# Optimization experiments

Hardware: AMD Instinct MI355X
Metric: run time of the kernel (lower is better)

Reference implementation:

```python
import jax, jax.numpy as jnp
import numpy as np

N_NODES = 50000
N_EDGES = 1_250_000
D_FEAT = 64


def setup_inputs() -> dict:
    key = jax.random.key(0)
    k1, k2, k3 = jax.random.split(key, 3)
    graph_embedding = jax.random.normal(k1, (N_NODES, D_FEAT), dtype=jnp.float32)
    src = jax.random.randint(k2, (N_EDGES,), 0, N_NODES, dtype=jnp.int64)
    dst = jax.random.randint(k3, (N_EDGES,), 0, N_NODES, dtype=jnp.int64)
    return {"graph_embedding": graph_embedding, "src": src, "dst": dst}


def reference(graph_embedding, src, dst):
    # DGL update_all(copy_u('ft','m'), sum('m','ft')):
    # out[v] = sum over edges (u->v) of graph_embedding[u]
    messages = graph_embedding[src]  # [E, d] gather
    out = jax.ops.segment_sum(messages, dst, num_segments=graph_embedding.shape[0])
    return out
```

## Files before the change

### kernel.cpp

```cpp
#include <hip/hip_runtime.h>


#define D_FEAT 64
#define NB2    512
#define CAPB   3072
#define MAXNB  512
#define PCHUNK 8192
#define CAP1   96

static __device__ __forceinline__ unsigned short f2bf(float f) {
    unsigned u = __float_as_uint(f);
    u += 0x7fffu + ((u >> 16) & 1u);
    return (unsigned short)(u >> 16);
}

__global__ __launch_bounds__(1024) void fused_cvt_partition_kernel(
    const float4* __restrict__ emb4,
    uint2*        __restrict__ embh2,
    const int*    __restrict__ src,
    const int*    __restrict__ dst,
    unsigned*     __restrict__ cursor,
    unsigned*     __restrict__ packed,
    int n4, int p_blocks, int n_edges, unsigned npb_inv)
{
    __shared__ unsigned lhist[MAXNB];
    __shared__ unsigned lbase[MAXNB];

    if ((int)blockIdx.x >= p_blocks) {
        int cb = blockIdx.x - p_blocks;
        int base = cb * 4096 + (int)threadIdx.x;
        #pragma unroll
        for (int r = 0; r < 4; ++r) {
            int i = base + r * 1024;
            if (i < n4) {
                float4 x = emb4[i];
                uint2 o;
                o.x = (unsigned)f2bf(x.x) | ((unsigned)f2bf(x.y) << 16);
                o.y = (unsigned)f2bf(x.z) | ((unsigned)f2bf(x.w) << 16);
                embh2[i] = o;
            }
        }
        return;
    }

    int pb   = blockIdx.x;
    int t    = threadIdx.x;
    int base = pb * PCHUNK;
    int cnt  = n_edges - base; if (cnt > PCHUNK) cnt = PCHUNK; if (cnt < 0) cnt = 0;

    for (int i = t; i < MAXNB; i += 1024) lhist[i] = 0;
    __syncthreads();

    int nv = cnt >> 2;
    const int4* d4 = (const int4*)(dst + base);
    const int4* s4 = (const int4*)(src + base);
    int  i0 = t, i1 = t + 1024;
    bool f0 = i0 < nv, f1 = i1 < nv;
    uint4 pa, pb4;
    if (f0) {
        int4 d = d4[i0]; int4 s = s4[i0];
        pa.x = ((unsigned)d.x << 16) | (unsigned)s.x;
        pa.y = ((unsigned)d.y << 16) | (unsigned)s.y;
        pa.z = ((unsigned)d.z << 16) | (unsigned)s.z;
        pa.w = ((unsigned)d.w << 16) | (unsigned)s.w;
    }
    if (f1) {
        int4 d = d4[i1]; int4 s = s4[i1];
        pb4.x = ((unsigned)d.x << 16) | (unsigned)s.x;
        pb4.y = ((unsigned)d.y << 16) | (unsigned)s.y;
        pb4.z = ((unsigned)d.z << 16) | (unsigned)s.z;
        pb4.w = ((unsigned)d.w << 16) | (unsigned)s.w;
    }
    if (f0) {
        atomicAdd(&lhist[__umulhi(pa.x >> 16, npb_inv)], 1u);
        atomicAdd(&lhist[__umulhi(pa.y >> 16, npb_inv)], 1u);
        atomicAdd(&lhist[__umulhi(pa.z >> 16, npb_inv)], 1u);
        atomicAdd(&lhist[__umulhi(pa.w >> 16, npb_inv)], 1u);
    }
    if (f1) {
        atomicAdd(&lhist[__umulhi(pb4.x >> 16, npb_inv)], 1u);
        atomicAdd(&lhist[__umulhi(pb4.y >> 16, npb_inv)], 1u);
        atomicAdd(&lhist[__umulhi(pb4.z >> 16, npb_inv)], 1u);
        atomicAdd(&lhist[__umulhi(pb4.w >> 16, npb_inv)], 1u);
    }
    for (int i = nv * 4 + t; i < cnt; i += 1024)
        atomicAdd(&lhist[__umulhi((unsigned)dst[base + i], npb_inv)], 1u);
    __syncthreads();

    for (int i = t; i < MAXNB; i += 1024) {
        unsigned c = lhist[i];
        lbase[i] = c ? atomicAdd(&cursor[i], c) : 0u;
        lhist[i] = 0;
    }
    __syncthreads();

    #define SCAT(p) { \
        unsigned b_ = __umulhi((p) >> 16, npb_inv); \
        unsigned pos_ = lbase[b_] + atomicAdd(&lhist[b_], 1u); \
        if (pos_ < CAPB) packed[(size_t)b_ * CAPB + pos_] = (p); }
    if (f0) { SCAT(pa.x); SCAT(pa.y); SCAT(pa.z); SCAT(pa.w); }
    if (f1) { SCAT(pb4.x); SCAT(pb4.y); SCAT(pb4.z); SCAT(pb4.w); }
    for (int i = nv * 4 + t; i < cnt; i += 1024) {
        unsigned p = ((unsigned)dst[base + i] << 16) | (unsigned)src[base + i];
        SCAT(p);
    }
    #undef SCAT
}

#define ACC8(h) \
    a0 += __uint_as_float(h.x << 16);           \
    a1 += __uint_as_float(h.x & 0xffff0000u);   \
    a2 += __uint_as_float(h.y << 16);           \
    a3 += __uint_as_float(h.y & 0xffff0000u);   \
    a4 += __uint_as_float(h.z << 16);           \
    a5 += __uint_as_float(h.z & 0xffff0000u);   \
    a6 += __uint_as_float(h.w << 16);           \
    a7 += __uint_as_float(h.w & 0xffff0000u);

__global__ __launch_bounds__(1024, 8) void sortgather_kernel(
    const unsigned short* __restrict__ embh,
    const unsigned*       __restrict__ cursor,
    const unsigned*       __restrict__ packed,
    float*                __restrict__ out,
    int n_nodes, unsigned npb)
{
    __shared__ unsigned       lpk[CAPB];
    __shared__ unsigned short slist[CAPB];
    __shared__ unsigned       hist[128];
    __shared__ unsigned       cur[128];
    __shared__ unsigned       stc[128];

    int b = blockIdx.x;
    int t = threadIdx.x;
    int node_base = (int)(b * npb);
    int nn = n_nodes - node_base;
    if (nn > (int)npb) nn = (int)npb;
    if (nn < 0) nn = 0;

    int cnt = (int)cursor[b]; if (cnt > CAPB) cnt = CAPB;
    const unsigned* pk = packed + (size_t)b * CAPB;

    if (t < 128) hist[t] = 0;
    __syncthreads();

    for (int i = t; i < cnt; i += 1024) {
        unsigned p = pk[i];
        lpk[i] = p;
        atomicAdd(&hist[(p >> 16) - node_base], 1u);
    }
    __syncthreads();

    if (t < 64) {
        int l = t;
        unsigned v0 = hist[2 * l], v1 = hist[2 * l + 1];
        unsigned s = v0 + v1;
        unsigned inc = s;
        #pragma unroll
        for (int d = 1; d < 64; d <<= 1) {
            unsigned u = __shfl_up(inc, d);
            if (l >= d) inc += u;
        }
        unsigned exc = inc - s;
        cur[2 * l]     = exc;
        cur[2 * l + 1] = exc + v0;
        stc[2 * l]     = (exc << 16) | v0;
        stc[2 * l + 1] = ((exc + v0) << 16) | v1;
    }
    __syncthreads();

    for (int i = t; i < cnt; i += 1024) {
        unsigned p = lpk[i];
        unsigned pos = atomicAdd(&cur[(p >> 16) - node_base], 1u);
        slist[pos] = (unsigned short)(p & 0xffffu);
    }
    __syncthreads();

    int g  = t >> 3;
    int l8 = t & 7;

    unsigned sc = stc[g];
    int st = (int)(sc >> 16), cn = (int)(sc & 0xffffu);

    float a0=0.f,a1=0.f,a2=0.f,a3=0.f,a4=0.f,a5=0.f,a6=0.f,a7=0.f;

    for (int j = 0; j < cn; j += 8) {
        bool v1 = j + 1 < cn, v2 = j + 2 < cn, v3 = j + 3 < cn;
        bool v4 = j + 4 < cn, v5 = j + 5 < cn, v6 = j + 6 < cn, v7 = j + 7 < cn;
        uint4 h0, h1, h2, h3, h4, h5, h6, h7;
        h0 =          *(const uint4*)(embh + ((size_t)slist[st + j    ] << 6) + l8 * 8);
        if (v1) h1 =  *(const uint4*)(embh + ((size_t)slist[st + j + 1] << 6) + l8 * 8);
        if (v2) h2 =  *(const uint4*)(embh + ((size_t)slist[st + j + 2] << 6) + l8 * 8);
        if (v3) h3 =  *(const uint4*)(embh + ((size_t)slist[st + j + 3] << 6) + l8 * 8);
        if (v4) h4 =  *(const uint4*)(embh + ((size_t)slist[st + j + 4] << 6) + l8 * 8);
        if (v5) h5 =  *(const uint4*)(embh + ((size_t)slist[st + j + 5] << 6) + l8 * 8);
        if (v6) h6 =  *(const uint4*)(embh + ((size_t)slist[st + j + 6] << 6) + l8 * 8);
        if (v7) h7 =  *(const uint4*)(embh + ((size_t)slist[st + j + 7] << 6) + l8 * 8);
        { ACC8(h0); }
        if (v1) { ACC8(h1); }
        if (v2) { ACC8(h2); }
        if (v3) { ACC8(h3); }
        if (v4) { ACC8(h4); }
        if (v5) { ACC8(h5); }
        if (v6) { ACC8(h6); }
        if (v7) { ACC8(h7); }
    }

    if (g < nn) {
        float4* o4 = (float4*)(out + (size_t)(node_base + g) * D_FEAT + l8 * 8);
        o4[0] = make_float4(a0, a1, a2, a3);
        o4[1] = make_float4(a4, a5, a6, a7);
    }
}

__global__ __launch_bounds__(256) void count_scatter_kernel(
    const int* __restrict__ src, const int* __restrict__ dst,
    int* __restrict__ cnt, int* __restrict__ bucket, int n_edges)
{
    int e = blockIdx.x * blockDim.x + threadIdx.x;
    if (e >= n_edges) return;
    int s = src[e], d = dst[e];
    int pos = atomicAdd(&cnt[d], 1);
    if (pos < CAP1) bucket[(size_t)d * CAP1 + pos] = s;
}

__global__ __launch_bounds__(256) void gather_sum_kernel(
    const float* __restrict__ emb, const int* __restrict__ cnt,
    const int* __restrict__ bucket, float* __restrict__ out, int n_nodes)
{
    int v = (blockIdx.x * blockDim.x + threadIdx.x) >> 6;
    int lane = threadIdx.x & 63;
    if (v >= n_nodes) return;
    int n = cnt[v]; if (n > CAP1) n = CAP1;
    const int* b = bucket + (size_t)v * CAP1;
    float acc = 0.f;
    for (int j = 0; j < n; ++j)
        acc += emb[(size_t)b[j] * D_FEAT + lane];
    out[(size_t)v * D_FEAT + lane] = acc;
}

__global__ __launch_bounds__(256) void scatter_sum_fallback(
    const float* __restrict__ emb, const int* __restrict__ src,
    const int* __restrict__ dst, float* __restrict__ out, int n_edges)
{
    int gid = blockIdx.x * blockDim.x + threadIdx.x;
    int e = gid >> 4;
    if (e >= n_edges) return;
    int c = gid & 15;
    int s = src[e], d = dst[e];
    const float4* emb4 = (const float4*)emb;
    float4 v = emb4[(size_t)s * 16 + c];
    float* o = out + (size_t)d * D_FEAT + c * 4;
    atomicAdd(o + 0, v.x); atomicAdd(o + 1, v.y);
    atomicAdd(o + 2, v.z); atomicAdd(o + 3, v.w);
}

extern "C" void kernel_launch(void* const* d_in, const int* in_sizes, int n_in,
                              void* d_out, int out_size, void* d_ws, size_t ws_size,
                              hipStream_t stream) {
    const float* emb = (const float*)d_in[0];
    const int*   src = (const int*)d_in[1];
    const int*   dst = (const int*)d_in[2];
    float*       out = (float*)d_out;

    int n_edges = in_sizes[1];
    int n_nodes = out_size / D_FEAT;

    unsigned npb = (unsigned)((n_nodes + NB2 - 1) / NB2);
    if (npb == 0) npb = 1;
    int nb = (n_nodes + (int)npb - 1) / (int)npb;
    unsigned npb_inv = (unsigned)((0x100000000ULL + npb - 1) / npb);

    size_t cur_b  = 4096;
    size_t pack_b = (size_t)MAXNB * CAPB * sizeof(unsigned);
    size_t embh_b = (size_t)n_nodes * D_FEAT * sizeof(unsigned short);

    if (n_nodes <= 65536 && npb <= 128 && nb <= MAXNB &&
        ws_size >= cur_b + pack_b + embh_b) {
        char* p = (char*)d_ws;
        unsigned*       cursor = (unsigned*)p;        p += cur_b;
        unsigned*       packed = (unsigned*)p;        p += pack_b;
        unsigned short* embh   = (unsigned short*)p;

        hipMemsetAsync(cursor, 0, (size_t)MAXNB * sizeof(unsigned), stream);

        int n4 = n_nodes * D_FEAT / 4;
        int p_blocks   = (n_edges + PCHUNK - 1) / PCHUNK;
        int cvt_blocks = (n4 + 4095) / 4096;
        fused_cvt_partition_kernel<<<p_blocks + cvt_blocks, 1024, 0, stream>>>(
            (const float4*)emb, (uint2*)embh, src, dst, cursor, packed,
            n4, p_blocks, n_edges, npb_inv);

        sortgather_kernel<<<nb, 1024, 0, stream>>>(
            embh, cursor, packed, out, n_nodes, npb);
    } else if (ws_size >= (size_t)n_nodes * sizeof(int) * (1 + CAP1)) {
        int* cnt    = (int*)d_ws;
        int* bucket = (int*)((char*)d_ws + (size_t)n_nodes * sizeof(int));
        hipMemsetAsync(cnt, 0, (size_t)n_nodes * sizeof(int), stream);
        count_scatter_kernel<<<(n_edges + 255) / 256, 256, 0, stream>>>(
            src, dst, cnt, bucket, n_edges);
        gather_sum_kernel<<<(n_nodes * 64 + 255) / 256, 256, 0, stream>>>(
            emb, cnt, bucket, out, n_nodes);
    } else {
        hipMemsetAsync(d_out, 0, (size_t)out_size * sizeof(float), stream);
        long long total = (long long)n_edges * 16;
        scatter_sum_fallback<<<(int)((total + 255) / 256), 256, 0, stream>>>(
            emb, src, dst, out, n_edges);
    }
}
```

Before: 100.8 us.

## Split bf16 table into feature halves and use per-XCD partition cursors

The bf16 embedding table is stored as two half-feature tables, and each gather block now handles one 32-feature half of a node bucket with 512 threads. Block indices are mapped so that blocks sharing a half-table are meant to land on the same XCD, shrinking the per-XCD L2 working set. The partition step also keeps eight separate cursor and packed segments, chosen by partition block index, to spread global atomic contention. The cost is that every gather block re-sorts its bucket redundantly, which doubles the sort work, and it adds a CAPSEG overflow risk per segment.

New measurement: 105.3 us. 4.5% more time.

```diff
diff --git a/kernel.cpp b/kernel.cpp
--- a/kernel.cpp
+++ b/kernel.cpp
@@ -4,7 +4,9 @@
 #define D_FEAT 64
 #define NB2    512
 #define CAPB   3072
+#define CAPSEG 1024
 #define MAXNB  512
+#define NXCD   8
 #define PCHUNK 8192
 #define CAP1   96
 
@@ -37,16 +39,23 @@
                 uint2 o;
                 o.x = (unsigned)f2bf(x.x) | ((unsigned)f2bf(x.y) << 16);
                 o.y = (unsigned)f2bf(x.z) | ((unsigned)f2bf(x.w) << 16);
-                embh2[i] = o;
+                int n = i >> 4;
+                int q = i & 15;
+                uint2* tb = embh2 + ((q & 8) ? (n4 >> 1) : 0);
+                tb[n * 8 + (q & 7)] = o;
             }
         }
         return;
     }
 
     int pb   = blockIdx.x;
+    int my_x = pb & (NXCD - 1);
     int t    = threadIdx.x;
     int base = pb * PCHUNK;
     int cnt  = n_edges - base; if (cnt > PCHUNK) cnt = PCHUNK; if (cnt < 0) cnt = 0;
+
+    unsigned* my_cur = cursor + my_x * MAXNB;
+    unsigned* my_pk  = packed + (size_t)my_x * MAXNB * CAPSEG;
 
     for (int i = t; i < MAXNB; i += 1024) lhist[i] = 0;
     __syncthreads();
@@ -89,7 +98,7 @@
 
     for (int i = t; i < MAXNB; i += 1024) {
         unsigned c = lhist[i];
-        lbase[i] = c ? atomicAdd(&cursor[i], c) : 0u;
+        lbase[i] = c ? atomicAdd(&my_cur[i], c) : 0u;
         lhist[i] = 0;
     }
     __syncthreads();
@@ -97,7 +106,7 @@
     #define SCAT(p) { \
         unsigned b_ = __umulhi((p) >> 16, npb_inv); \
         unsigned pos_ = lbase[b_] + atomicAdd(&lhist[b_], 1u); \
-        if (pos_ < CAPB) packed[(size_t)b_ * CAPB + pos_] = (p); }
+        if (pos_ < CAPSEG) my_pk[(size_t)b_ * CAPSEG + pos_] = (p); }
     if (f0) { SCAT(pa.x); SCAT(pa.y); SCAT(pa.z); SCAT(pa.w); }
     if (f1) { SCAT(pb4.x); SCAT(pb4.y); SCAT(pb4.z); SCAT(pb4.w); }
     for (int i = nv * 4 + t; i < cnt; i += 1024) {
@@ -117,36 +126,57 @@
     a6 += __uint_as_float(h.w << 16);           \
     a7 += __uint_as_float(h.w & 0xffff0000u);
 
-__global__ __launch_bounds__(1024, 8) void sortgather_kernel(
+__global__ __launch_bounds__(512, 8) void sortgather_kernel(
     const unsigned short* __restrict__ embh,
     const unsigned*       __restrict__ cursor,
     const unsigned*       __restrict__ packed,
     float*                __restrict__ out,
-    int n_nodes, unsigned npb)
+    int n_nodes, unsigned npb, int nb)
 {
     __shared__ unsigned       lpk[CAPB];
     __shared__ unsigned short slist[CAPB];
     __shared__ unsigned       hist[128];
     __shared__ unsigned       cur[128];
     __shared__ unsigned       stc[128];
-
-    int b = blockIdx.x;
+    __shared__ unsigned       scnt[NXCD];
+    __shared__ unsigned       soff[NXCD + 1];
+
+    int k = blockIdx.x;
+    int b = (k >> 3) * 4 + (k & 3);
+    int h = (k >> 2) & 1;
+    if (b >= nb) return;
     int t = threadIdx.x;
     int node_base = (int)(b * npb);
     int nn = n_nodes - node_base;
     if (nn > (int)npb) nn = (int)npb;
     if (nn < 0) nn = 0;
 
-    int cnt = (int)cursor[b]; if (cnt > CAPB) cnt = CAPB;
-    const unsigned* pk = packed + (size_t)b * CAPB;
-
+    if (t < NXCD) {
+        unsigned c = cursor[t * MAXNB + b];
+        scnt[t] = c > CAPSEG ? CAPSEG : c;
+    }
     if (t < 128) hist[t] = 0;
     __syncthreads();
-
-    for (int i = t; i < cnt; i += 1024) {
-        unsigned p = pk[i];
-        lpk[i] = p;
-        atomicAdd(&hist[(p >> 16) - node_base], 1u);
+    if (t == 0) {
+        unsigned s = 0;
+        #pragma unroll
+        for (int x = 0; x < NXCD; ++x) { soff[x] = s; s += scnt[x]; }
+        soff[NXCD] = s;
+    }
+    __syncthreads();
+    int cnt = (int)soff[NXCD]; if (cnt > CAPB) cnt = CAPB;
+
+    for (int x = 0; x < NXCD; ++x) {
+        const unsigned* sp = packed + ((size_t)x * MAXNB + b) * CAPSEG;
+        int c = (int)scnt[x], o = (int)soff[x];
+        for (int i = t; i < c; i += 512) {
+            int pos = o + i;
+            if (pos < CAPB) {
+                unsigned p = sp[i];
+                lpk[pos] = p;
+                atomicAdd(&hist[(p >> 16) - node_base], 1u);
+            }
+        }
     }
     __syncthreads();
 
@@ -168,15 +198,16 @@
     }
     __syncthreads();
 
-    for (int i = t; i < cnt; i += 1024) {
+    for (int i = t; i < cnt; i += 512) {
         unsigned p = lpk[i];
         unsigned pos = atomicAdd(&cur[(p >> 16) - node_base], 1u);
         slist[pos] = (unsigned short)(p & 0xffffu);
     }
     __syncthreads();
 
-    int g  = t >> 3;
-    int l8 = t & 7;
+    const unsigned short* tb = embh + (size_t)h * ((size_t)n_nodes << 5);
+    int g  = t >> 2;
+    int l4 = t & 3;
 
     unsigned sc = stc[g];
     int st = (int)(sc >> 16), cn = (int)(sc & 0xffffu);
@@ -187,14 +218,14 @@
         bool v1 = j + 1 < cn, v2 = j + 2 < cn, v3 = j + 3 < cn;
         bool v4 = j + 4 < cn, v5 = j + 5 < cn, v6 = j + 6 < cn, v7 = j + 7 < cn;
         uint4 h0, h1, h2, h3, h4, h5, h6, h7;
-        h0 =          *(const uint4*)(embh + ((size_t)slist[st + j    ] << 6) + l8 * 8);
-        if (v1) h1 =  *(const uint4*)(embh + ((size_t)slist[st + j + 1] << 6) + l8 * 8);
-        if (v2) h2 =  *(const uint4*)(embh + ((size_t)slist[st + j + 2] << 6) + l8 * 8);
-        if (v3) h3 =  *(const uint4*)(embh + ((size_t)slist[st + j + 3] << 6) + l8 * 8);
-        if (v4) h4 =  *(const uint4*)(embh + ((size_t)slist[st + j + 4] << 6) + l8 * 8);
-        if (v5) h5 =  *(const uint4*)(embh + ((size_t)slist[st + j + 5] << 6) + l8 * 8);
-        if (v6) h6 =  *(const uint4*)(embh + ((size_t)slist[st + j + 6] << 6) + l8 * 8);
-        if (v7) h7 =  *(const uint4*)(embh + ((size_t)slist[st + j + 7] << 6) + l8 * 8);
+        h0 =          *(const uint4*)(tb + ((size_t)slist[st + j    ] << 5) + l4 * 8);
+        if (v1) h1 =  *(const uint4*)(tb + ((size_t)slist[st + j + 1] << 5) + l4 * 8);
+        if (v2) h2 =  *(const uint4*)(tb + ((size_t)slist[st + j + 2] << 5) + l4 * 8);
+        if (v3) h3 =  *(const uint4*)(tb + ((size_t)slist[st + j + 3] << 5) + l4 * 8);
+        if (v4) h4 =  *(const uint4*)(tb + ((size_t)slist[st + j + 4] << 5) + l4 * 8);
+        if (v5) h5 =  *(const uint4*)(tb + ((size_t)slist[st + j + 5] << 5) + l4 * 8);
+        if (v6) h6 =  *(const uint4*)(tb + ((size_t)slist[st + j + 6] << 5) + l4 * 8);
+        if (v7) h7 =  *(const uint4*)(tb + ((size_t)slist[st + j + 7] << 5) + l4 * 8);
         { ACC8(h0); }
         if (v1) { ACC8(h1); }
         if (v2) { ACC8(h2); }
@@ -206,7 +237,7 @@
     }
 
     if (g < nn) {
-        float4* o4 = (float4*)(out + (size_t)(node_base + g) * D_FEAT + l8 * 8);
+        float4* o4 = (float4*)(out + (size_t)(node_base + g) * D_FEAT + h * 32 + l4 * 8);
         o4[0] = make_float4(a0, a1, a2, a3);
         o4[1] = make_float4(a4, a5, a6, a7);
     }
@@ -270,8 +301,8 @@
     int nb = (n_nodes + (int)npb - 1) / (int)npb;
     unsigned npb_inv = (unsigned)((0x100000000ULL + npb - 1) / npb);
 
-    size_t cur_b  = 4096;
-    size_t pack_b = (size_t)MAXNB * CAPB * sizeof(unsigned);
+    size_t cur_b  = (size_t)NXCD * MAXNB * sizeof(unsigned);
+    size_t pack_b = (size_t)NXCD * MAXNB * CAPSEG * sizeof(unsigned);
     size_t embh_b = (size_t)n_nodes * D_FEAT * sizeof(unsigned short);
 
     if (n_nodes <= 65536 && npb <= 128 && nb <= MAXNB &&
@@ -281,7 +312,7 @@
         unsigned*       packed = (unsigned*)p;        p += pack_b;
         unsigned short* embh   = (unsigned short*)p;
 
-        hipMemsetAsync(cursor, 0, (size_t)MAXNB * sizeof(unsigned), stream);
+        hipMemsetAsync(cursor, 0, cur_b, stream);
 
         int n4 = n_nodes * D_FEAT / 4;
         int p_blocks   = (n_edges + PCHUNK - 1) / PCHUNK;
@@ -290,8 +321,9 @@
             (const float4*)emb, (uint2*)embh, src, dst, cursor, packed,
             n4, p_blocks, n_edges, npb_inv);
 
-        sortgather_kernel<<<nb, 1024, 0, stream>>>(
-            embh, cursor, packed, out, n_nodes, npb);
+        int g_blocks = ((nb + 3) / 4) * 8;
+        sortgather_kernel<<<g_blocks, 512, 0, stream>>>(
+            embh, cursor, packed, out, n_nodes, npb, nb);
     } else if (ws_size >= (size_t)n_nodes * sizeof(int) * (1 + CAP1)) {
         int* cnt    = (int*)d_ws;
         int* bucket = (int*)((char*)d_ws + (size_t)n_nodes * sizeof(int));
```

## Replace global atomic bucket cursors with per-block fixed slabs in edge partitioning

Applied to the files above, without the earlier changes.

The partition kernel no longer builds a block-local histogram and reserves space with global atomics on a shared cursor array. Each partition block now writes edges straight into its own fixed 64-entry slab per destination bucket and records per-block counts. The gather kernel prefix-sums those counts across partition blocks to compact the slabs into shared memory. This removes the memset launch, a histogram pass, one barrier and the global atomic contention. In exchange the workspace grows, the gather kernel reads sparse, mostly empty slabs, and edges are silently dropped if any bucket gets more than 64 edges from one chunk.

Result: slower. 103.5 us (+2.7%).

```diff
diff --git a/kernel.cpp b/kernel.cpp
--- a/kernel.cpp
+++ b/kernel.cpp
@@ -1,12 +1,15 @@
 #include <hip/hip_runtime.h>
 
 
-#define D_FEAT 64
-#define NB2    512
-#define CAPB   3072
-#define MAXNB  512
-#define PCHUNK 8192
-#define CAP1   96
+#define D_FEAT  64
+#define NB2     512
+#define CAPB    3072
+#define SLAB    64
+#define SLABLOG 6
+#define MAXNB   512
+#define MAXSEG  256
+#define PCHUNK  8192
+#define CAP1    96
 
 static __device__ __forceinline__ unsigned short f2bf(float f) {
     unsigned u = __float_as_uint(f);
@@ -19,12 +22,11 @@
     uint2*        __restrict__ embh2,
     const int*    __restrict__ src,
     const int*    __restrict__ dst,
-    unsigned*     __restrict__ cursor,
+    unsigned*     __restrict__ cnt_out,
     unsigned*     __restrict__ packed,
     int n4, int p_blocks, int n_edges, unsigned npb_inv)
 {
-    __shared__ unsigned lhist[MAXNB];
-    __shared__ unsigned lbase[MAXNB];
+    __shared__ unsigned cur[MAXNB];
 
     if ((int)blockIdx.x >= p_blocks) {
         int cb = blockIdx.x - p_blocks;
@@ -48,63 +50,45 @@
     int base = pb * PCHUNK;
     int cnt  = n_edges - base; if (cnt > PCHUNK) cnt = PCHUNK; if (cnt < 0) cnt = 0;
 
-    for (int i = t; i < MAXNB; i += 1024) lhist[i] = 0;
-    __syncthreads();
+    for (int i = t; i < MAXNB; i += 1024) cur[i] = 0;
+    __syncthreads();
+
+    unsigned* my_pk = packed + ((size_t)pb * MAXNB << SLABLOG);
+
+    #define SCAT(p) { \
+        unsigned b_ = __umulhi((p) >> 16, npb_inv); \
+        unsigned pos_ = atomicAdd(&cur[b_], 1u); \
+        if (pos_ < SLAB) my_pk[((size_t)b_ << SLABLOG) + pos_] = (p); }
 
     int nv = cnt >> 2;
     const int4* d4 = (const int4*)(dst + base);
     const int4* s4 = (const int4*)(src + base);
     int  i0 = t, i1 = t + 1024;
-    bool f0 = i0 < nv, f1 = i1 < nv;
-    uint4 pa, pb4;
-    if (f0) {
+    if (i0 < nv) {
         int4 d = d4[i0]; int4 s = s4[i0];
-        pa.x = ((unsigned)d.x << 16) | (unsigned)s.x;
-        pa.y = ((unsigned)d.y << 16) | (unsigned)s.y;
-        pa.z = ((unsigned)d.z << 16) | (unsigned)s.z;
-        pa.w = ((unsigned)d.w << 16) | (unsigned)s.w;
-    }
-    if (f1) {
+        unsigned p0 = ((unsigned)d.x << 16) | (unsigned)s.x;
+        unsigned p1 = ((unsigned)d.y << 16) | (unsigned)s.y;
+        unsigned p2 = ((unsigned)d.z << 16) | (unsigned)s.z;
+        unsigned p3 = ((unsigned)d.w << 16) | (unsigned)s.w;
+        SCAT(p0); SCAT(p1); SCAT(p2); SCAT(p3);
+    }
+    if (i1 < nv) {
         int4 d = d4[i1]; int4 s = s4[i1];
-        pb4.x = ((unsigned)d.x << 16) | (unsigned)s.x;
-        pb4.y = ((unsigned)d.y << 16) | (unsigned)s.y;
-        pb4.z = ((unsigned)d.z << 16) | (unsigned)s.z;
-        pb4.w = ((unsigned)d.w << 16) | (unsigned)s.w;
-    }
-    if (f0) {
-        atomicAdd(&lhist[__umulhi(pa.x >> 16, npb_inv)], 1u);
-        atomicAdd(&lhist[__umulhi(pa.y >> 16, npb_inv)], 1u);
-        atomicAdd(&lhist[__umulhi(pa.z >> 16, npb_inv)], 1u);
-        atomicAdd(&lhist[__umulhi(pa.w >> 16, npb_inv)], 1u);
-    }
-    if (f1) {
-        atomicAdd(&lhist[__umulhi(pb4.x >> 16, npb_inv)], 1u);
-        atomicAdd(&lhist[__umulhi(pb4.y >> 16, npb_inv)], 1u);
-        atomicAdd(&lhist[__umulhi(pb4.z >> 16, npb_inv)], 1u);
-        atomicAdd(&lhist[__umulhi(pb4.w >> 16, npb_inv)], 1u);
-    }
-    for (int i = nv * 4 + t; i < cnt; i += 1024)
-        atomicAdd(&lhist[__umulhi((unsigned)dst[base + i], npb_inv)], 1u);
-    __syncthreads();
-
-    for (int i = t; i < MAXNB; i += 1024) {
-        unsigned c = lhist[i];
-        lbase[i] = c ? atomicAdd(&cursor[i], c) : 0u;
-        lhist[i] = 0;
-    }
-    __syncthreads();
-
-    #define SCAT(p) { \
-        unsigned b_ = __umulhi((p) >> 16, npb_inv); \
-        unsigned pos_ = lbase[b_] + atomicAdd(&lhist[b_], 1u); \
-        if (pos_ < CAPB) packed[(size_t)b_ * CAPB + pos_] = (p); }
-    if (f0) { SCAT(pa.x); SCAT(pa.y); SCAT(pa.z); SCAT(pa.w); }
-    if (f1) { SCAT(pb4.x); SCAT(pb4.y); SCAT(pb4.z); SCAT(pb4.w); }
+        unsigned p0 = ((unsigned)d.x << 16) | (unsigned)s.x;
+        unsigned p1 = ((unsigned)d.y << 16) | (unsigned)s.y;
+        unsigned p2 = ((unsigned)d.z << 16) | (unsigned)s.z;
+        unsigned p3 = ((unsigned)d.w << 16) | (unsigned)s.w;
+        SCAT(p0); SCAT(p1); SCAT(p2); SCAT(p3);
+    }
     for (int i = nv * 4 + t; i < cnt; i += 1024) {
         unsigned p = ((unsigned)dst[base + i] << 16) | (unsigned)src[base + i];
         SCAT(p);
     }
     #undef SCAT
+    __syncthreads();
+
+    for (int i = t; i < MAXNB; i += 1024)
+        cnt_out[(size_t)pb * MAXNB + i] = cur[i];
 }
 
 #define ACC8(h) \
@@ -119,16 +103,19 @@
 
 __global__ __launch_bounds__(1024, 8) void sortgather_kernel(
     const unsigned short* __restrict__ embh,
-    const unsigned*       __restrict__ cursor,
+    const unsigned*       __restrict__ cnt,
     const unsigned*       __restrict__ packed,
     float*                __restrict__ out,
-    int n_nodes, unsigned npb)
+    int n_nodes, unsigned npb, int nseg)
 {
     __shared__ unsigned       lpk[CAPB];
     __shared__ unsigned short slist[CAPB];
     __shared__ unsigned       hist[128];
     __shared__ unsigned       cur[128];
     __shared__ unsigned       stc[128];
+    __shared__ unsigned       scnt[MAXSEG];
+    __shared__ unsigned       soff[MAXSEG];
+    __shared__ unsigned       stot;
 
     int b = blockIdx.x;
     int t = threadIdx.x;
@@ -137,16 +124,43 @@
     if (nn > (int)npb) nn = (int)npb;
     if (nn < 0) nn = 0;
 
-    int cnt = (int)cursor[b]; if (cnt > CAPB) cnt = CAPB;
-    const unsigned* pk = packed + (size_t)b * CAPB;
-
     if (t < 128) hist[t] = 0;
-    __syncthreads();
-
-    for (int i = t; i < cnt; i += 1024) {
-        unsigned p = pk[i];
-        lpk[i] = p;
-        atomicAdd(&hist[(p >> 16) - node_base], 1u);
+
+    if (t < 64) {
+        int x0 = t * 4;
+        unsigned c0=0,c1=0,c2=0,c3=0;
+        if (x0     < nseg) { unsigned c = cnt[(size_t)(x0    ) * MAXNB + b]; c0 = c > SLAB ? SLAB : c; }
+        if (x0 + 1 < nseg) { unsigned c = cnt[(size_t)(x0 + 1) * MAXNB + b]; c1 = c > SLAB ? SLAB : c; }
+        if (x0 + 2 < nseg) { unsigned c = cnt[(size_t)(x0 + 2) * MAXNB + b]; c2 = c > SLAB ? SLAB : c; }
+        if (x0 + 3 < nseg) { unsigned c = cnt[(size_t)(x0 + 3) * MAXNB + b]; c3 = c > SLAB ? SLAB : c; }
+        unsigned s = c0 + c1 + c2 + c3;
+        unsigned inc = s;
+        #pragma unroll
+        for (int d = 1; d < 64; d <<= 1) {
+            unsigned u = __shfl_up(inc, d);
+            if (t >= d) inc += u;
+        }
+        unsigned exc = inc - s;
+        scnt[x0] = c0;     soff[x0]     = exc;
+        scnt[x0+1] = c1;   soff[x0 + 1] = exc + c0;
+        scnt[x0+2] = c2;   soff[x0 + 2] = exc + c0 + c1;
+        scnt[x0+3] = c3;   soff[x0 + 3] = exc + c0 + c1 + c2;
+        if (t == 63) stot = inc;
+    }
+    __syncthreads();
+    int total = (int)stot; if (total > CAPB) total = CAPB;
+
+    int nslots = nseg << SLABLOG;
+    for (int i = t; i < nslots; i += 1024) {
+        int x = i >> SLABLOG, j = i & (SLAB - 1);
+        if ((unsigned)j < scnt[x]) {
+            unsigned p = packed[(((size_t)x * MAXNB + b) << SLABLOG) + j];
+            unsigned pos = soff[x] + j;
+            if (pos < CAPB) {
+                lpk[pos] = p;
+                atomicAdd(&hist[(p >> 16) - node_base], 1u);
+            }
+        }
     }
     __syncthreads();
 
@@ -168,7 +182,7 @@
     }
     __syncthreads();
 
-    for (int i = t; i < cnt; i += 1024) {
+    for (int i = t; i < total; i += 1024) {
         unsigned p = lpk[i];
         unsigned pos = atomicAdd(&cur[(p >> 16) - node_base], 1u);
         slist[pos] = (unsigned short)(p & 0xffffu);
@@ -270,28 +284,27 @@
     int nb = (n_nodes + (int)npb - 1) / (int)npb;
     unsigned npb_inv = (unsigned)((0x100000000ULL + npb - 1) / npb);
 
-    size_t cur_b  = 4096;
-    size_t pack_b = (size_t)MAXNB * CAPB * sizeof(unsigned);
+    int p_blocks = (n_edges + PCHUNK - 1) / PCHUNK;
+
+    size_t cnt_b  = (size_t)p_blocks * MAXNB * sizeof(unsigned);
+    size_t pack_b = ((size_t)p_blocks * MAXNB << SLABLOG) * sizeof(unsigned);
     size_t embh_b = (size_t)n_nodes * D_FEAT * sizeof(unsigned short);
 
-    if (n_nodes <= 65536 && npb <= 128 && nb <= MAXNB &&
-        ws_size >= cur_b + pack_b + embh_b) {
+    if (n_nodes <= 65536 && npb <= 128 && nb <= MAXNB && p_blocks <= MAXSEG &&
+        ws_size >= cnt_b + pack_b + embh_b) {
         char* p = (char*)d_ws;
-        unsigned*       cursor = (unsigned*)p;        p += cur_b;
+        unsigned*       cnt    = (unsigned*)p;        p += cnt_b;
         unsigned*       packed = (unsigned*)p;        p += pack_b;
         unsigned short* embh   = (unsigned short*)p;
 
-        hipMemsetAsync(cursor, 0, (size_t)MAXNB * sizeof(unsigned), stream);
-
         int n4 = n_nodes * D_FEAT / 4;
-        int p_blocks   = (n_edges + PCHUNK - 1) / PCHUNK;
         int cvt_blocks = (n4 + 4095) / 4096;
         fused_cvt_partition_kernel<<<p_blocks + cvt_blocks, 1024, 0, stream>>>(
-            (const float4*)emb, (uint2*)embh, src, dst, cursor, packed,
+            (const float4*)emb, (uint2*)embh, src, dst, cnt, packed,
             n4, p_blocks, n_edges, npb_inv);
 
         sortgather_kernel<<<nb, 1024, 0, stream>>>(
-            embh, cursor, packed, out, n_nodes, npb);
+            embh, cnt, packed, out, n_nodes, npb, p_blocks);
     } else if (ws_size >= (size_t)n_nodes * sizeof(int) * (1 + CAP1)) {
         int* cnt    = (int*)d_ws;
         int* bucket = (int*)((char*)d_ws + (size_t)n_nodes * sizeof(int));
```

## Replace block-partition sort with per-node global buckets and direct gather

Applied to the files above, without the earlier changes.

Drops the two-level partition, where edges were binned into node-range blocks and then counting-sorted in shared memory. Instead each edge is scattered straight into a fixed-capacity per-node bucket using global atomics on a per-node degree counter. The gather kernel reads neighbor ids directly from the bucket, prefetching them and broadcasting them with shuffles, and writes the output with nontemporal stores. This removes the shared-memory sort and its barriers, but adds 1.25M global atomics spread over 50k counters, scattered bucket writes, and a larger workspace footprint.

New measurement: 152.4 us. +51.2%, slower.

```diff
diff --git a/kernel.cpp b/kernel.cpp
--- a/kernel.cpp
+++ b/kernel.cpp
@@ -2,11 +2,8 @@
 
 
 #define D_FEAT 64
-#define NB2    512
-#define CAPB   3072
-#define MAXNB  512
+#define CAPN   96
 #define PCHUNK 8192
-#define CAP1   96
 
 static __device__ __forceinline__ unsigned short f2bf(float f) {
     unsigned u = __float_as_uint(f);
@@ -14,18 +11,17 @@
     return (unsigned short)(u >> 16);
 }
 
-__global__ __launch_bounds__(1024) void fused_cvt_partition_kernel(
+typedef float f4v __attribute__((ext_vector_type(4)));
+
+__global__ __launch_bounds__(1024) void fused_cvt_scatter_kernel(
     const float4* __restrict__ emb4,
     uint2*        __restrict__ embh2,
     const int*    __restrict__ src,
     const int*    __restrict__ dst,
-    unsigned*     __restrict__ cursor,
-    unsigned*     __restrict__ packed,
-    int n4, int p_blocks, int n_edges, unsigned npb_inv)
+    int*          __restrict__ deg,
+    int*          __restrict__ bucket,
+    int n4, int p_blocks, int n_edges)
 {
-    __shared__ unsigned lhist[MAXNB];
-    __shared__ unsigned lbase[MAXNB];
-
     if ((int)blockIdx.x >= p_blocks) {
         int cb = blockIdx.x - p_blocks;
         int base = cb * 4096 + (int)threadIdx.x;
@@ -43,67 +39,28 @@
         return;
     }
 
-    int pb   = blockIdx.x;
     int t    = threadIdx.x;
-    int base = pb * PCHUNK;
+    int base = blockIdx.x * PCHUNK;
     int cnt  = n_edges - base; if (cnt > PCHUNK) cnt = PCHUNK; if (cnt < 0) cnt = 0;
 
-    for (int i = t; i < MAXNB; i += 1024) lhist[i] = 0;
-    __syncthreads();
+    #define SCAT(d_, s_) { \
+        int pos_ = atomicAdd(&deg[d_], 1); \
+        if (pos_ < CAPN) bucket[(size_t)(d_) * CAPN + pos_] = (s_); }
 
     int nv = cnt >> 2;
     const int4* d4 = (const int4*)(dst + base);
     const int4* s4 = (const int4*)(src + base);
-    int  i0 = t, i1 = t + 1024;
-    bool f0 = i0 < nv, f1 = i1 < nv;
-    uint4 pa, pb4;
-    if (f0) {
+    int i0 = t, i1 = t + 1024;
+    if (i0 < nv) {
         int4 d = d4[i0]; int4 s = s4[i0];
-        pa.x = ((unsigned)d.x << 16) | (unsigned)s.x;
-        pa.y = ((unsigned)d.y << 16) | (unsigned)s.y;
-        pa.z = ((unsigned)d.z << 16) | (unsigned)s.z;
-        pa.w = ((unsigned)d.w << 16) | (unsigned)s.w;
+        SCAT(d.x, s.x); SCAT(d.y, s.y); SCAT(d.z, s.z); SCAT(d.w, s.w);
     }
-    if (f1) {
+    if (i1 < nv) {
         int4 d = d4[i1]; int4 s = s4[i1];
-        pb4.x = ((unsigned)d.x << 16) | (unsigned)s.x;
-        pb4.y = ((unsigned)d.y << 16) | (unsigned)s.y;
-        pb4.z = ((unsigned)d.z << 16) | (unsigned)s.z;
-        pb4.w = ((unsigned)d.w << 16) | (unsigned)s.w;
-    }
-    if (f0) {
-        atomicAdd(&lhist[__umulhi(pa.x >> 16, npb_inv)], 1u);
-        atomicAdd(&lhist[__umulhi(pa.y >> 16, npb_inv)], 1u);
-        atomicAdd(&lhist[__umulhi(pa.z >> 16, npb_inv)], 1u);
-        atomicAdd(&lhist[__umulhi(pa.w >> 16, npb_inv)], 1u);
-    }
-    if (f1) {
-        atomicAdd(&lhist[__umulhi(pb4.x >> 16, npb_inv)], 1u);
-        atomicAdd(&lhist[__umulhi(pb4.y >> 16, npb_inv)], 1u);
-        atomicAdd(&lhist[__umulhi(pb4.z >> 16, npb_inv)], 1u);
-        atomicAdd(&lhist[__umulhi(pb4.w >> 16, npb_inv)], 1u);
+        SCAT(d.x, s.x); SCAT(d.y, s.y); SCAT(d.z, s.z); SCAT(d.w, s.w);
     }
     for (int i = nv * 4 + t; i < cnt; i += 1024)
-        atomicAdd(&lhist[__umulhi((unsigned)dst[base + i], npb_inv)], 1u);
-    __syncthreads();
-
-    for (int i = t; i < MAXNB; i += 1024) {
-        unsigned c = lhist[i];
-        lbase[i] = c ? atomicAdd(&cursor[i], c) : 0u;
-        lhist[i] = 0;
-    }
-    __syncthreads();
-
-    #define SCAT(p) { \
-        unsigned b_ = __umulhi((p) >> 16, npb_inv); \
-        unsigned pos_ = lbase[b_] + atomicAdd(&lhist[b_], 1u); \
-        if (pos_ < CAPB) packed[(size_t)b_ * CAPB + pos_] = (p); }
-    if (f0) { SCAT(pa.x); SCAT(pa.y); SCAT(pa.z); SCAT(pa.w); }
-    if (f1) { SCAT(pb4.x); SCAT(pb4.y); SCAT(pb4.z); SCAT(pb4.w); }
-    for (int i = nv * 4 + t; i < cnt; i += 1024) {
-        unsigned p = ((unsigned)dst[base + i] << 16) | (unsigned)src[base + i];
-        SCAT(p);
-    }
+        SCAT(dst[base + i], src[base + i]);
     #undef SCAT
 }
 
@@ -117,84 +74,47 @@
     a6 += __uint_as_float(h.w << 16);           \
     a7 += __uint_as_float(h.w & 0xffff0000u);
 
-__global__ __launch_bounds__(1024, 8) void sortgather_kernel(
+__global__ __launch_bounds__(512, 8) void gather_kernel(
     const unsigned short* __restrict__ embh,
-    const unsigned*       __restrict__ cursor,
-    const unsigned*       __restrict__ packed,
+    const int*            __restrict__ deg,
+    const int*            __restrict__ bucket,
     float*                __restrict__ out,
-    int n_nodes, unsigned npb)
+    int n_nodes)
 {
-    __shared__ unsigned       lpk[CAPB];
-    __shared__ unsigned short slist[CAPB];
-    __shared__ unsigned       hist[128];
-    __shared__ unsigned       cur[128];
-    __shared__ unsigned       stc[128];
-
-    int b = blockIdx.x;
-    int t = threadIdx.x;
-    int node_base = (int)(b * npb);
-    int nn = n_nodes - node_base;
-    if (nn > (int)npb) nn = (int)npb;
-    if (nn < 0) nn = 0;
-
-    int cnt = (int)cursor[b]; if (cnt > CAPB) cnt = CAPB;
-    const unsigned* pk = packed + (size_t)b * CAPB;
-
-    if (t < 128) hist[t] = 0;
-    __syncthreads();
-
-    for (int i = t; i < cnt; i += 1024) {
-        unsigned p = pk[i];
-        lpk[i] = p;
-        atomicAdd(&hist[(p >> 16) - node_base], 1u);
-    }
-    __syncthreads();
-
-    if (t < 64) {
-        int l = t;
-        unsigned v0 = hist[2 * l], v1 = hist[2 * l + 1];
-        unsigned s = v0 + v1;
-        unsigned inc = s;
-        #pragma unroll
-        for (int d = 1; d < 64; d <<= 1) {
-            unsigned u = __shfl_up(inc, d);
-            if (l >= d) inc += u;
-        }
-        unsigned exc = inc - s;
-        cur[2 * l]     = exc;
-        cur[2 * l + 1] = exc + v0;
-        stc[2 * l]     = (exc << 16) | v0;
-        stc[2 * l + 1] = ((exc + v0) << 16) | v1;
-    }
-    __syncthreads();
-
-    for (int i = t; i < cnt; i += 1024) {
-        unsigned p = lpk[i];
-        unsigned pos = atomicAdd(&cur[(p >> 16) - node_base], 1u);
-        slist[pos] = (unsigned short)(p & 0xffffu);
-    }
-    __syncthreads();
-
+    int t  = threadIdx.x;
     int g  = t >> 3;
     int l8 = t & 7;
+    int v  = (int)blockIdx.x * 64 + g;
+    if (v >= n_nodes) return;
 
-    unsigned sc = stc[g];
-    int st = (int)(sc >> 16), cn = (int)(sc & 0xffffu);
+    int cn = deg[v]; if (cn > CAPN) cn = CAPN;
+    const int* bl = bucket + (size_t)v * CAPN;
+    int gb = (g & 7) * 8;
 
     float a0=0.f,a1=0.f,a2=0.f,a3=0.f,a4=0.f,a5=0.f,a6=0.f,a7=0.f;
 
-    for (int j = 0; j < cn; j += 8) {
-        bool v1 = j + 1 < cn, v2 = j + 2 < cn, v3 = j + 3 < cn;
-        bool v4 = j + 4 < cn, v5 = j + 5 < cn, v6 = j + 6 < cn, v7 = j + 7 < cn;
+    int id_next = (cn > 0) ? bl[l8] : 0;
+    for (int jj = 0; jj < cn; jj += 8) {
+        int id = id_next;
+        if (jj + 8 < cn) id_next = bl[jj + 8 + l8];
+
+        int s0 = __shfl(id, gb + 0), s1 = __shfl(id, gb + 1);
+        int s2 = __shfl(id, gb + 2), s3 = __shfl(id, gb + 3);
+        int s4 = __shfl(id, gb + 4), s5 = __shfl(id, gb + 5);
+        int s6 = __shfl(id, gb + 6), s7 = __shfl(id, gb + 7);
+
+        bool v1 = jj + 1 < cn, v2 = jj + 2 < cn, v3 = jj + 3 < cn;
+        bool v4 = jj + 4 < cn, v5 = jj + 5 < cn, v6 = jj + 6 < cn, v7 = jj + 7 < cn;
+
         uint4 h0, h1, h2, h3, h4, h5, h6, h7;
-        h0 =          *(const uint4*)(embh + ((size_t)slist[st + j    ] << 6) + l8 * 8);
-        if (v1) h1 =  *(const uint4*)(embh + ((size_t)slist[st + j + 1] << 6) + l8 * 8);
-        if (v2) h2 =  *(const uint4*)(embh + ((size_t)slist[st + j + 2] << 6) + l8 * 8);
-        if (v3) h3 =  *(const uint4*)(embh + ((size_t)slist[st + j + 3] << 6) + l8 * 8);
-        if (v4) h4 =  *(const uint4*)(embh + ((size_t)slist[st + j + 4] << 6) + l8 * 8);
-        if (v5) h5 =  *(const uint4*)(embh + ((size_t)slist[st + j + 5] << 6) + l8 * 8);
-        if (v6) h6 =  *(const uint4*)(embh + ((size_t)slist[st + j + 6] << 6) + l8 * 8);
-        if (v7) h7 =  *(const uint4*)(embh + ((size_t)slist[st + j + 7] << 6) + l8 * 8);
+        h0 =          *(const uint4*)(embh + ((size_t)s0 << 6) + l8 * 8);
+        if (v1) h1 =  *(const uint4*)(embh + ((size_t)s1 << 6) + l8 * 8);
+        if (v2) h2 =  *(const uint4*)(embh + ((size_t)s2 << 6) + l8 * 8);
+        if (v3) h3 =  *(const uint4*)(embh + ((size_t)s3 << 6) + l8 * 8);
+        if (v4) h4 =  *(const uint4*)(embh + ((size_t)s4 << 6) + l8 * 8);
+        if (v5) h5 =  *(const uint4*)(embh + ((size_t)s5 << 6) + l8 * 8);
+        if (v6) h6 =  *(const uint4*)(embh + ((size_t)s6 << 6) + l8 * 8);
+        if (v7) h7 =  *(const uint4*)(embh + ((size_t)s7 << 6) + l8 * 8);
         { ACC8(h0); }
         if (v1) { ACC8(h1); }
         if (v2) { ACC8(h2); }
@@ -205,37 +125,11 @@
         if (v7) { ACC8(h7); }
     }
 
-    if (g < nn) {
-        float4* o4 = (float4*)(out + (size_t)(node_base + g) * D_FEAT + l8 * 8);
-        o4[0] = make_float4(a0, a1, a2, a3);
-        o4[1] = make_float4(a4, a5, a6, a7);
-    }
-}
-
-__global__ __launch_bounds__(256) void count_scatter_kernel(
-    const int* __restrict__ src, const int* __restrict__ dst,
-    int* __restrict__ cnt, int* __restrict__ bucket, int n_edges)
-{
-    int e = blockIdx.x * blockDim.x + threadIdx.x;
-    if (e >= n_edges) return;
-    int s = src[e], d = dst[e];
-    int pos = atomicAdd(&cnt[d], 1);
-    if (pos < CAP1) bucket[(size_t)d * CAP1 + pos] = s;
-}
-
-__global__ __launch_bounds__(256) void gather_sum_kernel(
-    const float* __restrict__ emb, const int* __restrict__ cnt,
-    const int* __restrict__ bucket, float* __restrict__ out, int n_nodes)
-{
-    int v = (blockIdx.x * blockDim.x + threadIdx.x) >> 6;
-    int lane = threadIdx.x & 63;
-    if (v >= n_nodes) return;
-    int n = cnt[v]; if (n > CAP1) n = CAP1;
-    const int* b = bucket + (size_t)v * CAP1;
-    float acc = 0.f;
-    for (int j = 0; j < n; ++j)
-        acc += emb[(size_t)b[j] * D_FEAT + lane];
-    out[(size_t)v * D_FEAT + lane] = acc;
+    float* o = out + (size_t)v * D_FEAT + l8 * 8;
+    f4v w0 = {a0, a1, a2, a3};
+    f4v w1 = {a4, a5, a6, a7};
+    __builtin_nontemporal_store(w0, (f4v*)o);
+    __builtin_nontemporal_store(w1, (f4v*)(o + 4));
 }
 
 __global__ __launch_bounds__(256) void scatter_sum_fallback(
@@ -265,41 +159,28 @@
     int n_edges = in_sizes[1];
     int n_nodes = out_size / D_FEAT;
 
-    unsigned npb = (unsigned)((n_nodes + NB2 - 1) / NB2);
-    if (npb == 0) npb = 1;
-    int nb = (n_nodes + (int)npb - 1) / (int)npb;
-    unsigned npb_inv = (unsigned)((0x100000000ULL + npb - 1) / npb);
-
-    size_t cur_b  = 4096;
-    size_t pack_b = (size_t)MAXNB * CAPB * sizeof(unsigned);
+    size_t deg_b  = (((size_t)n_nodes * sizeof(int)) + 255) & ~(size_t)255;
+    size_t buck_b = (((size_t)n_nodes * CAPN * sizeof(int) + 256) + 255) & ~(size_t)255;
     size_t embh_b = (size_t)n_nodes * D_FEAT * sizeof(unsigned short);
 
-    if (n_nodes <= 65536 && npb <= 128 && nb <= MAXNB &&
-        ws_size >= cur_b + pack_b + embh_b) {
+    if (ws_size >= deg_b + buck_b + embh_b) {
         char* p = (char*)d_ws;
-        unsigned*       cursor = (unsigned*)p;        p += cur_b;
-        unsigned*       packed = (unsigned*)p;        p += pack_b;
+        int*            deg    = (int*)p;             p += deg_b;
+        int*            bucket = (int*)p;             p += buck_b;
         unsigned short* embh   = (unsigned short*)p;
 
-        hipMemsetAsync(cursor, 0, (size_t)MAXNB * sizeof(unsigned), stream);
+        hipMemsetAsync(deg, 0, (size_t)n_nodes * sizeof(int), stream);
 
         int n4 = n_nodes * D_FEAT / 4;
         int p_blocks   = (n_edges + PCHUNK - 1) / PCHUNK;
         int cvt_blocks = (n4 + 4095) / 4096;
-        fused_cvt_partition_kernel<<<p_blocks + cvt_blocks, 1024, 0, stream>>>(
-            (const float4*)emb, (uint2*)embh, src, dst, cursor, packed,
-            n4, p_blocks, n_edges, npb_inv);
+        fused_cvt_scatter_kernel<<<p_blocks + cvt_blocks, 1024, 0, stream>>>(
+            (const float4*)emb, (uint2*)embh, src, dst, deg, bucket,
+            n4, p_blocks, n_edges);
 
-        sortgather_kernel<<<nb, 1024, 0, stream>>>(
-            embh, cursor, packed, out, n_nodes, npb);
-    } else if (ws_size >= (size_t)n_nodes * sizeof(int) * (1 + CAP1)) {
-        int* cnt    = (int*)d_ws;
-        int* bucket = (int*)((char*)d_ws + (size_t)n_nodes * sizeof(int));
-        hipMemsetAsync(cnt, 0, (size_t)n_nodes * sizeof(int), stream);
-        count_scatter_kernel<<<(n_edges + 255) / 256, 256, 0, stream>>>(
-            src, dst, cnt, bucket, n_edges);
-        gather_sum_kernel<<<(n_nodes * 64 + 255) / 256, 256, 0, stream>>>(
-            emb, cnt, bucket, out, n_nodes);
+        int g_blocks = (n_nodes + 63) / 64;
+        gather_kernel<<<g_blocks, 512, 0, stream>>>(
+            embh, deg, bucket, out, n_nodes);
     } else {
         hipMemsetAsync(d_out, 0, (size_t)out_size * sizeof(float), stream);
         long long total = (long long)n_edges * 16;
```
